# Optimization experiments

Measured on AMD Instinct MI355X. Metric: run time of the kernel, lower is better.

The kernel has to match this reference:

```python
import jax, jax.numpy as jnp
import numpy as np

B, S, D, H, FF = 4, 2048, 1024, 16, 4096
DT, TARGET, ITERS = 0.1, 0.0, 5


def _ln(x, w, b):
    mu = jnp.mean(x, axis=-1, keepdims=True)
    var = jnp.mean((x - mu) ** 2, axis=-1, keepdims=True)
    return (x - mu) * jax.lax.rsqrt(var + 1e-5) * w + b


def setup_inputs() -> dict:
    key = jax.random.key(0)
    ks = iter(jax.random.split(key, 16))
    w = lambda shape: jax.random.normal(next(ks), shape, dtype=jnp.float32) * 0.02
    return {
        "x": jax.random.normal(next(ks), (B, S, D), dtype=jnp.float32),
        "ln_attn_w": jnp.ones((D,), jnp.float32), "ln_attn_b": jnp.zeros((D,), jnp.float32),
        "attn_in_w": w((3 * D, D)), "attn_in_b": jnp.zeros((3 * D,), jnp.float32),
        "attn_out_w": w((D, D)), "attn_out_b": jnp.zeros((D,), jnp.float32),
        "ln1_w": jnp.ones((D,), jnp.float32), "ln1_b": jnp.zeros((D,), jnp.float32),
        "ln2_w": jnp.ones((D,), jnp.float32), "ln2_b": jnp.zeros((D,), jnp.float32),
        "inl_u_w": w((D, D)), "inl_u_b": jnp.zeros((D,), jnp.float32),
        "inl_a_w": w((D, D)), "inl_a_b": jnp.zeros((D,), jnp.float32),
        "inl_b_w": w((D, D)), "inl_b_b": jnp.zeros((D,), jnp.float32),
        "inl_g_w": w((D, D)), "inl_g_b": jnp.zeros((D,), jnp.float32),
        "ff1_w": w((FF, D)), "ff1_b": jnp.zeros((FF,), jnp.float32),
        "ff2_w": w((D, FF)), "ff2_b": jnp.zeros((D,), jnp.float32),
    }


def reference(x, ln_attn_w, ln_attn_b, attn_in_w, attn_in_b, attn_out_w, attn_out_b,
              ln1_w, ln1_b, ln2_w, ln2_b,
              inl_u_w, inl_u_b, inl_a_w, inl_a_b, inl_b_w, inl_b_b, inl_g_w, inl_g_b,
              ff1_w, ff1_b, ff2_w, ff2_b):
    dh = D // H
    scale = 1.0 / np.sqrt(dh).astype(np.float32)
    # --- causal multi-head attention (dropout = identity, eval mode) ---
    xn = _ln(x, ln_attn_w, ln_attn_b)
    qkv = xn @ attn_in_w.T + attn_in_b            # [B,S,3D]
    q, k, v = jnp.split(qkv, 3, axis=-1)
    hsplit = lambda t: t.reshape(B, S, H, dh).transpose(0, 2, 1, 3)  # [B,H,S,dh]
    q, k, v = hsplit(q), hsplit(k), hsplit(v)
    scores = jnp.einsum('bhqd,bhkd->bhqk', q, k) * scale
    causal = jnp.triu(jnp.ones((S, S), dtype=bool), 1)
    scores = jnp.where(causal, jnp.finfo(scores.dtype).min, scores)
    probs = jax.nn.softmax(scores, axis=-1)
    attn_out = jnp.einsum('bhqk,bhkd->bhqd', probs, v).transpose(0, 2, 1, 3).reshape(B, S, D)
    attn_out = attn_out @ attn_out_w.T + attn_out_b
    x = x + attn_out
    context = attn_out
    # --- INL integrator dynamics (controllers depend only on context) ---
    xs = _ln(x, ln1_w, ln1_b)
    vs = jnp.zeros_like(xs)
    u = context @ inl_u_w.T + inl_u_b
    alpha = jax.nn.sigmoid(context @ inl_a_w.T + inl_a_b)
    beta = jax.nn.softplus(context @ inl_b_w.T + inl_b_b)
    g = jax.nn.sigmoid(context @ inl_g_w.T + inl_g_b)
    for _ in range(ITERS):
        vs = vs + DT * (alpha * (TARGET - xs) - beta * vs + u)
        xs = xs + DT * g * vs
    x = x + xs
    # --- feed-forward (exact GELU as torch default) ---
    h = _ln(x, ln2_w, ln2_b)
    x = x + (jax.nn.gelu(h @ ff1_w.T + ff1_b, approximate=False) @ ff2_w.T + ff2_b)
    return x
```

## Files before the change

kernel.cpp:

```cpp
#include <hip/hip_runtime.h>
#include <cstdint>
#include <cmath>

typedef __attribute__((ext_vector_type(4))) float floatx4;
typedef __attribute__((ext_vector_type(8))) __bf16 bf16x8;
typedef __attribute__((ext_vector_type(4))) unsigned short ushort4v;

#define DEVI static __device__ __forceinline__

DEVI unsigned short f2b(float f) {
    unsigned x = __float_as_uint(f);
    return (unsigned short)((x + 0x7fffu + ((x >> 16) & 1u)) >> 16);
}
DEVI float b2f(unsigned short u) { return __uint_as_float(((unsigned)u) << 16); }

DEVI void load16(void* lds, const void* g) {
    __builtin_amdgcn_global_load_lds(
        (__attribute__((address_space(1))) void*)(const_cast<void*>(g)),
        (__attribute__((address_space(3))) void*)lds, 16, 0, 0);
}

DEVI floatx4 MFMA16(bf16x8 a, bf16x8 b, floatx4 c) {
    return __builtin_amdgcn_mfma_f32_16x16x32_bf16(a, b, c, 0, 0, 0);
}

__global__ __launch_bounds__(256) void cvt_all(const float* __restrict__ s0,
                                               const float* __restrict__ s1,
                                               const float* __restrict__ s2,
                                               const float* __restrict__ s3,
                                               const float* __restrict__ s4,
                                               const float* __restrict__ s5,
                                               const float* __restrict__ s6,
                                               const float* __restrict__ s7,
                                               unsigned short* d0, unsigned short* d1,
                                               unsigned short* d2, unsigned short* d3,
                                               unsigned short* d4, unsigned short* d5,
                                               unsigned short* d6, unsigned short* d7) {
    int i = blockIdx.x * 256 + threadIdx.x;
    int seg = i >> 18;
    int j = i & 262143;
    const float* src; unsigned short* dst;
    if (seg < 3)        { src = s0; dst = d0; j += seg * 262144; }
    else if (seg == 3)  { src = s1; dst = d1; }
    else if (seg == 4)  { src = s2; dst = d2; }
    else if (seg == 5)  { src = s3; dst = d3; }
    else if (seg == 6)  { src = s4; dst = d4; }
    else if (seg == 7)  { src = s5; dst = d5; }
    else if (seg < 12)  { src = s6; dst = d6; j += (seg - 8) * 262144; }
    else                { src = s7; dst = d7; j += (seg - 12) * 262144; }
    floatx4 v = ((const floatx4*)src)[j];
    ushort4v o;
    o[0] = f2b(v[0]); o[1] = f2b(v[1]); o[2] = f2b(v[2]); o[3] = f2b(v[3]);
    ((ushort4v*)dst)[j] = o;
}

__global__ __launch_bounds__(256) void catbias_kernel(const float* __restrict__ a,
                                                      const float* __restrict__ b,
                                                      const float* __restrict__ c,
                                                      const float* __restrict__ d,
                                                      float* __restrict__ o) {
    int i = blockIdx.x * 256 + threadIdx.x;
    int p = i >> 10, j = i & 1023;
    float v = (p == 0) ? a[j] : (p == 1) ? b[j] : (p == 2) ? c[j] : d[j];
    o[i] = v;
}

__global__ __launch_bounds__(256) void ln_kernel(const float* __restrict__ in,
                                                 const float* __restrict__ w,
                                                 const float* __restrict__ b,
                                                 unsigned short* __restrict__ obf) {
    const int row = blockIdx.x, tid = threadIdx.x;
    const floatx4* pr = (const floatx4*)(in + (size_t)row * 1024);
    floatx4 v = pr[tid];
    float s  = v[0] + v[1] + v[2] + v[3];
    float ss = v[0]*v[0] + v[1]*v[1] + v[2]*v[2] + v[3]*v[3];
    #pragma unroll
    for (int o = 32; o >= 1; o >>= 1) { s += __shfl_xor(s, o); ss += __shfl_xor(ss, o); }
    __shared__ float red[8];
    int wv = tid >> 6, lane = tid & 63;
    if (lane == 0) { red[wv] = s; red[4 + wv] = ss; }
    __syncthreads();
    s  = red[0] + red[1] + red[2] + red[3];
    ss = red[4] + red[5] + red[6] + red[7];
    float mu  = s * (1.0f / 1024.0f);
    float var = ss * (1.0f / 1024.0f) - mu * mu;
    float rstd = rsqrtf(var + 1e-5f);
    floatx4 wv4 = ((const floatx4*)w)[tid];
    floatx4 bv4 = ((const floatx4*)b)[tid];
    ushort4v t;
    #pragma unroll
    for (int c = 0; c < 4; c++) t[c] = f2b((v[c] - mu) * rstd * wv4[c] + bv4[c]);
    ((ushort4v*)(obf + (size_t)row * 1024))[tid] = t;
}

__global__ __launch_bounds__(256) void integrator_ln_kernel(const float* __restrict__ w1,
                                                            const float* __restrict__ b1,
                                                            const float* __restrict__ w2,
                                                            const float* __restrict__ b2,
                                                            const unsigned short* __restrict__ uabg,
                                                            float* __restrict__ xio,
                                                            unsigned short* __restrict__ hb) {
    const int row = blockIdx.x, tid = threadIdx.x;
    const int wv = tid >> 6, lane = tid & 63;
    __shared__ float red[8], red2[8];

    floatx4 v = ((const floatx4*)(xio + (size_t)row * 1024))[tid];
    float s  = v[0] + v[1] + v[2] + v[3];
    float ss = v[0]*v[0] + v[1]*v[1] + v[2]*v[2] + v[3]*v[3];
    #pragma unroll
    for (int o = 32; o >= 1; o >>= 1) { s += __shfl_xor(s, o); ss += __shfl_xor(ss, o); }
    if (lane == 0) { red[wv] = s; red[4 + wv] = ss; }
    __syncthreads();
    s  = red[0] + red[1] + red[2] + red[3];
    ss = red[4] + red[5] + red[6] + red[7];
    float mu  = s * (1.0f / 1024.0f);
    float rstd = rsqrtf(ss * (1.0f / 1024.0f) - mu * mu + 1e-5f);
    floatx4 w1v = ((const floatx4*)w1)[tid];
    floatx4 b1v = ((const floatx4*)b1)[tid];

    const unsigned short* ubase = uabg + (size_t)row * 4096 + tid * 4;
    ushort4v uu = *(const ushort4v*)(ubase);
    ushort4v aa = *(const ushort4v*)(ubase + 1024);
    ushort4v bb = *(const ushort4v*)(ubase + 2048);
    ushort4v gg = *(const ushort4v*)(ubase + 3072);
    floatx4 res;
    #pragma unroll
    for (int c = 0; c < 4; c++) {
        float xs = (v[c] - mu) * rstd * w1v[c] + b1v[c];
        float u = b2f(uu[c]), a = b2f(aa[c]), bt = b2f(bb[c]), g = b2f(gg[c]);
        float vs = 0.f;
        #pragma unroll
        for (int t = 0; t < 5; t++) {
            vs += 0.1f * (-a * xs - bt * vs + u);
            xs += 0.1f * g * vs;
        }
        res[c] = v[c] + xs;
    }
    ((floatx4*)(xio + (size_t)row * 1024))[tid] = res;

    float s2  = res[0] + res[1] + res[2] + res[3];
    float ss2 = res[0]*res[0] + res[1]*res[1] + res[2]*res[2] + res[3]*res[3];
    #pragma unroll
    for (int o = 32; o >= 1; o >>= 1) { s2 += __shfl_xor(s2, o); ss2 += __shfl_xor(ss2, o); }
    if (lane == 0) { red2[wv] = s2; red2[4 + wv] = ss2; }
    __syncthreads();
    s2  = red2[0] + red2[1] + red2[2] + red2[3];
    ss2 = red2[4] + red2[5] + red2[6] + red2[7];
    float mu2  = s2 * (1.0f / 1024.0f);
    float rstd2 = rsqrtf(ss2 * (1.0f / 1024.0f) - mu2 * mu2 + 1e-5f);
    floatx4 w2v = ((const floatx4*)w2)[tid];
    floatx4 b2v = ((const floatx4*)b2)[tid];
    ushort4v t;
    #pragma unroll
    for (int c = 0; c < 4; c++) t[c] = f2b((res[c] - mu2) * rstd2 * w2v[c] + b2v[c]);
    ((ushort4v*)(hb + (size_t)row * 1024))[tid] = t;
}

template <int EPI>
__global__ __launch_bounds__(256, 3) void gemm_bt(const unsigned short* __restrict__ A,
                                                  const unsigned short* __restrict__ W,
                                                  const float* __restrict__ bias, int K,
                                                  unsigned short* __restrict__ ob0,
                                                  unsigned short* __restrict__ ob1,
                                                  unsigned short* __restrict__ ob2,
                                                  float* __restrict__ of0,
                                                  const float* __restrict__ xres) {
    __shared__ unsigned short sA[3][128 * 32];
    __shared__ unsigned short sB[3][128 * 32];
    const int tid = threadIdx.x;
    const int wave = tid >> 6, lane = tid & 63;
    const int ln = lane & 15, quad = lane >> 4;
    const size_t m0 = (size_t)blockIdx.y * 128;
    const int n0 = blockIdx.x * 128;
    const int wm = (wave >> 1) * 64, wn = (wave & 1) * 64;

    const floatx4 z4 = {0.f, 0.f, 0.f, 0.f};
    floatx4 acc[4][4];
    #pragma unroll
    for (int mt = 0; mt < 4; mt++)
        #pragma unroll
        for (int nt = 0; nt < 4; nt++) acc[mt][nt] = z4;

    const int r16 = lane >> 2;
    const int gsw = (((lane & 3) ^ (r16 & 3) ^ ((r16 >> 2) & 3))) * 8;
    const int arow = wave * 16 + r16;
    const unsigned short* gA = A + (m0 + (size_t)arow) * K + gsw;
    const unsigned short* gB = W + ((size_t)(n0 + arow)) * K + gsw;
    const size_t rs64 = (size_t)64 * K;
    const int so = wave * 512;
    const int swr = ((quad ^ (ln & 3) ^ ((ln >> 2) & 3))) * 8;

    const int T = K >> 5;

    load16(&sA[0][so], gA);
    load16(&sA[0][so + 2048], gA + rs64);
    load16(&sB[0][so], gB);
    load16(&sB[0][so + 2048], gB + rs64);
    load16(&sA[1][so], gA + 32);
    load16(&sA[1][so + 2048], gA + rs64 + 32);
    load16(&sB[1][so], gB + 32);
    load16(&sB[1][so + 2048], gB + rs64 + 32);
    asm volatile("s_waitcnt vmcnt(4)" ::: "memory");
    asm volatile("s_barrier" ::: "memory");

    bf16x8 fa0[4], fb0[4], fa1[4], fb1[4];
    #pragma unroll
    for (int mt = 0; mt < 4; mt++)
        fa0[mt] = *(const bf16x8*)&sA[0][(wm + mt * 16 + ln) * 32 + swr];
    #pragma unroll
    for (int nt = 0; nt < 4; nt++)
        fb0[nt] = *(const bf16x8*)&sB[0][(wn + nt * 16 + ln) * 32 + swr];

    auto step = [&](int t, bf16x8* afc, bf16x8* bfc, bf16x8* afn, bf16x8* bfn) {
        if (t + 2 < T) {
            const int k = (t + 2) * 32;
            const int nb = (t + 2) % 3;
            load16(&sA[nb][so], gA + k);
            load16(&sA[nb][so + 2048], gA + rs64 + k);
            load16(&sB[nb][so], gB + k);
            load16(&sB[nb][so + 2048], gB + rs64 + k);
        }
        __builtin_amdgcn_sched_barrier(0);
        __builtin_amdgcn_s_setprio(1);
        #pragma unroll
        for (int mt = 0; mt < 4; mt++)
            #pragma unroll
            for (int nt = 0; nt < 4; nt++)
                acc[mt][nt] = MFMA16(afc[mt], bfc[nt], acc[mt][nt]);
        __builtin_amdgcn_s_setprio(0);
        __builtin_amdgcn_sched_barrier(0);
        if (t + 1 < T) {
            if (t + 2 < T) {
                asm volatile("s_waitcnt vmcnt(4) lgkmcnt(0)" ::: "memory");
            } else {
                asm volatile("s_waitcnt vmcnt(0) lgkmcnt(0)" ::: "memory");
            }
            asm volatile("s_barrier" ::: "memory");
            const int nb = (t + 1) % 3;
            afn[0] = *(const bf16x8*)&sA[nb][(wm + ln) * 32 + swr];
            #pragma unroll
            for (int nt = 0; nt < 4; nt++)
                bfn[nt] = *(const bf16x8*)&sB[nb][(wn + nt * 16 + ln) * 32 + swr];
            #pragma unroll
            for (int mt = 1; mt < 4; mt++)
                afn[mt] = *(const bf16x8*)&sA[nb][(wm + mt * 16 + ln) * 32 + swr];
        }
    };

    #pragma unroll 1
    for (int t = 0; t < T; t += 2) {
        step(t, fa0, fb0, fa1, fb1);
        step(t + 1, fa1, fb1, fa0, fb0);
    }

    const size_t rowb = m0 + wm + quad * 4;
    const int colb = n0 + wn + ln;
    #pragma unroll
    for (int mt = 0; mt < 4; mt++) {
        #pragma unroll
        for (int nt = 0; nt < 4; nt++) {
            const int n = colb + nt * 16;
            const float bs = bias[n];
            #pragma unroll
            for (int r = 0; r < 4; r++) {
                const size_t row = rowb + mt * 16 + r;
                float c = acc[mt][nt][r] + bs;
                if constexpr (EPI == 0) {
                    int sect = n >> 10, d1 = n & 1023, h = d1 >> 6, d = d1 & 63;
                    int bb = (int)(row >> 11), s = (int)(row & 2047);
                    size_t bh = (size_t)(bb * 16 + h);
                    if (sect == 0)      ob0[(bh * 2048 + s) * 64 + d] = f2b(c);
                    else if (sect == 1) ob1[(bh * 2048 + s) * 64 + d] = f2b(c);
                    else                ob2[(bh * 64 + d) * 2048 + s] = f2b(c);
                } else if constexpr (EPI == 1) {
                    size_t idx = row * 1024 + n;
                    ob0[idx] = f2b(c);
                    of0[idx] = xres[idx] + c;
                } else if constexpr (EPI == 2) {
                    int p = n >> 10;
                    float v;
                    if (p == 0)       v = c;
                    else if (p == 2)  v = fmaxf(c, 0.f) + log1pf(__expf(-fabsf(c)));
                    else              v = 1.f / (1.f + __expf(-c));
                    ob0[row * 4096 + n] = f2b(v);
                } else if constexpr (EPI == 3) {
                    float v = 0.5f * c * (1.f + erff(c * 0.70710678118654752f));
                    ob0[row * 4096 + n] = f2b(v);
                } else {
                    size_t idx = row * 1024 + n;
                    of0[idx] += c;
                }
            }
        }
    }
}

#define PSTR 72
__global__ __launch_bounds__(256, 3) void attn_kernel(const unsigned short* __restrict__ Qb,
                                                      const unsigned short* __restrict__ Kb,
                                                      const unsigned short* __restrict__ Vtb,
                                                      unsigned short* __restrict__ Ob) {
    __shared__ unsigned short sK[2][64 * 64];
    __shared__ unsigned short sVt[2][64 * 64];
    __shared__ unsigned short sQP[128 * PSTR];
    const int pr = blockIdx.x;
    const int bh = blockIdx.y;
    const int tid = threadIdx.x, wave = tid >> 6, lane = tid & 63;
    const int ln = lane & 15, quad = lane >> 4;
    const unsigned short* Q  = Qb  + (size_t)bh * 2048 * 64;
    const unsigned short* Kp = Kb  + (size_t)bh * 2048 * 64;
    const unsigned short* Vt = Vtb + (size_t)bh * 64 * 2048;

    const int rl  = lane >> 3;
    const int gsw = (((lane & 7) ^ rl)) * 8;
    const int sseg = wave * 2;
    const unsigned short* kbase = Kp + (size_t)(sseg * 8 + rl) * 64 + gsw;
    const unsigned short* vbase = Vt + (size_t)(sseg * 8 + rl) * 2048 + gsw;
    unsigned short* sP = &sQP[wave * 32 * PSTR];
    const int bb = bh >> 4, h = bh & 15;
    const floatx4 z4 = {0.f, 0.f, 0.f, 0.f};

    #pragma unroll 1
    for (int phase = 0; phase < 2; phase++) {
        const int qt = phase ? pr : (15 - pr);
        const int q0 = qt * 128;
        const int T = 2 * qt + 2;

        #pragma unroll
        for (int i = 0; i < 4; i++) {
            int s = wave * 4 + i;
            load16(&sQP[s * 512], Q + (size_t)(q0 + s * 8 + rl) * 64 + gsw);
        }
        load16(&sK[0][sseg * 512], kbase);
        load16(&sK[0][(sseg + 1) * 512], kbase + (size_t)8 * 64);
        load16(&sVt[0][sseg * 512], vbase);
        load16(&sVt[0][(sseg + 1) * 512], vbase + (size_t)8 * 2048);
        asm volatile("s_waitcnt vmcnt(0)" ::: "memory");
        asm volatile("s_barrier" ::: "memory");

        bf16x8 aq[2][2];
        #pragma unroll
        for (int mt = 0; mt < 2; mt++)
            #pragma unroll
            for (int ks = 0; ks < 2; ks++)
                aq[mt][ks] = *(const bf16x8*)&sQP[(wave * 32 + mt * 16 + ln) * 64 +
                                                  (((ks * 4 + quad) ^ (ln & 7)) * 8)];
        asm volatile("s_waitcnt lgkmcnt(0)" ::: "memory");
        asm volatile("s_barrier" ::: "memory");

        floatx4 Oacc[2][4];
        float m_run[2][4], l_run[2][4];
        #pragma unroll
        for (int mt = 0; mt < 2; mt++)
            #pragma unroll
            for (int j = 0; j < 4; j++) { Oacc[mt][j] = z4; m_run[mt][j] = -1e30f; l_run[mt][j] = 0.f; }

        const int wave_first = q0 + wave * 32;
        const int wave_last  = wave_first + 31;

        #pragma unroll 1
        for (int t = 0; t < T; t++) {
            const int kk0 = t * 64;
            const int cur = t & 1;
            if (t + 1 < T) {
                const unsigned short* kg = kbase + (size_t)(kk0 + 64) * 64;
                const unsigned short* vg = vbase + (size_t)(kk0 + 64);
                load16(&sK[cur ^ 1][sseg * 512], kg);
                load16(&sK[cur ^ 1][(sseg + 1) * 512], kg + (size_t)8 * 64);
                load16(&sVt[cur ^ 1][sseg * 512], vg);
                load16(&sVt[cur ^ 1][(sseg + 1) * 512], vg + (size_t)8 * 2048);
                asm volatile("s_waitcnt vmcnt(4)" ::: "memory");
            } else {
                asm volatile("s_waitcnt vmcnt(0)" ::: "memory");
            }
            asm volatile("s_barrier" ::: "memory");

            if (kk0 <= wave_last) {
                floatx4 Sc[2][4];
                #pragma unroll
                for (int mt = 0; mt < 2; mt++)
                    #pragma unroll
                    for (int nt = 0; nt < 4; nt++) Sc[mt][nt] = z4;
                __builtin_amdgcn_s_setprio(1);
                #pragma unroll
                for (int ks = 0; ks < 2; ks++) {
                    #pragma unroll
                    for (int nt = 0; nt < 4; nt++) {
                        bf16x8 bk = *(const bf16x8*)&sK[cur][(nt * 16 + ln) * 64 +
                                                             (((ks * 4 + quad) ^ (ln & 7)) * 8)];
                        #pragma unroll
                        for (int mt = 0; mt < 2; mt++)
                            Sc[mt][nt] = MFMA16(aq[mt][ks], bk, Sc[mt][nt]);
                    }
                }
                __builtin_amdgcn_s_setprio(0);
                const bool diag = (kk0 + 63 > wave_first);
                #pragma unroll
                for (int mt = 0; mt < 2; mt++)
                    #pragma unroll
                    for (int nt = 0; nt < 4; nt++)
                        #pragma unroll
                        for (int r = 0; r < 4; r++) {
                            float v = Sc[mt][nt][r] * 0.125f;
                            if (diag) {
                                int rowg = wave_first + mt * 16 + quad * 4 + r;
                                int colg = kk0 + nt * 16 + ln;
                                if (colg > rowg) v = -1e30f;
                            }
                            Sc[mt][nt][r] = v;
                        }
                float alpha[2][4];
                #pragma unroll
                for (int mt = 0; mt < 2; mt++)
                    #pragma unroll
                    for (int r = 0; r < 4; r++) {
                        float mx = fmaxf(fmaxf(Sc[mt][0][r], Sc[mt][1][r]), fmaxf(Sc[mt][2][r], Sc[mt][3][r]));
                        #pragma unroll
                        for (int off = 1; off < 16; off <<= 1) mx = fmaxf(mx, __shfl_xor(mx, off));
                        float mnew = fmaxf(m_run[mt][r], mx);
                        alpha[mt][r] = __expf(m_run[mt][r] - mnew);
                        m_run[mt][r] = mnew;
                    }
                #pragma unroll
                for (int mt = 0; mt < 2; mt++)
                    #pragma unroll
                    for (int r = 0; r < 4; r++) {
                        float rs = 0.f;
                        #pragma unroll
                        for (int nt = 0; nt < 4; nt++) {
                            float p = __expf(Sc[mt][nt][r] - m_run[mt][r]);
                            Sc[mt][nt][r] = p;
                            rs += p;
                        }
                        #pragma unroll
                        for (int off = 1; off < 16; off <<= 1) rs += __shfl_xor(rs, off);
                        l_run[mt][r] = l_run[mt][r] * alpha[mt][r] + rs;
                    }
                #pragma unroll
                for (int mt = 0; mt < 2; mt++)
                    #pragma unroll
                    for (int nt = 0; nt < 4; nt++)
                        #pragma unroll
                        for (int r = 0; r < 4; r++) Oacc[mt][nt][r] *= alpha[mt][r];
                #pragma unroll
                for (int mt = 0; mt < 2; mt++)
                    #pragma unroll
                    for (int nt = 0; nt < 4; nt++)
                        #pragma unroll
                        for (int r = 0; r < 4; r++)
                            sP[(mt * 16 + quad * 4 + r) * PSTR + nt * 16 + ln] = f2b(Sc[mt][nt][r]);
                __builtin_amdgcn_s_setprio(1);
                #pragma unroll
                for (int kp = 0; kp < 2; kp++) {
                    bf16x8 ap[2];
                    #pragma unroll
                    for (int mt = 0; mt < 2; mt++)
                        ap[mt] = *(const bf16x8*)&sP[(mt * 16 + ln) * PSTR + kp * 32 + quad * 8];
                    #pragma unroll
                    for (int nt = 0; nt < 4; nt++) {
                        bf16x8 bv = *(const bf16x8*)&sVt[cur][(nt * 16 + ln) * 64 +
                                                              (((kp * 4 + quad) ^ (ln & 7)) * 8)];
                        #pragma unroll
                        for (int mt = 0; mt < 2; mt++)
                            Oacc[mt][nt] = MFMA16(ap[mt], bv, Oacc[mt][nt]);
                    }
                }
                __builtin_amdgcn_s_setprio(0);
            }
            asm volatile("s_barrier" ::: "memory");
        }

        #pragma unroll
        for (int mt = 0; mt < 2; mt++)
            #pragma unroll
            for (int nt = 0; nt < 4; nt++)
                #pragma unroll
                for (int r = 0; r < 4; r++) {
                    float o = Oacc[mt][nt][r] / l_run[mt][r];
                    int srow = q0 + wave * 32 + mt * 16 + quad * 4 + r;
                    size_t tok = (size_t)bb * 2048 + srow;
                    Ob[tok * 1024 + h * 64 + nt * 16 + ln] = f2b(o);
                }
    }
}

extern "C" void kernel_launch(void* const* d_in, const int* in_sizes, int n_in,
                              void* d_out, int out_size, void* d_ws, size_t ws_size,
                              hipStream_t stream) {
    const float* x          = (const float*)d_in[0];
    const float* ln_attn_w  = (const float*)d_in[1];
    const float* ln_attn_b  = (const float*)d_in[2];
    const float* attn_in_w  = (const float*)d_in[3];
    const float* attn_in_b  = (const float*)d_in[4];
    const float* attn_out_w = (const float*)d_in[5];
    const float* attn_out_b = (const float*)d_in[6];
    const float* ln1_w      = (const float*)d_in[7];
    const float* ln1_b      = (const float*)d_in[8];
    const float* ln2_w      = (const float*)d_in[9];
    const float* ln2_b      = (const float*)d_in[10];
    const float* inl_u_w    = (const float*)d_in[11];
    const float* inl_u_b    = (const float*)d_in[12];
    const float* inl_a_w    = (const float*)d_in[13];
    const float* inl_a_b    = (const float*)d_in[14];
    const float* inl_b_w    = (const float*)d_in[15];
    const float* inl_b_b    = (const float*)d_in[16];
    const float* inl_g_w    = (const float*)d_in[17];
    const float* inl_g_b    = (const float*)d_in[18];
    const float* ff1_w      = (const float*)d_in[19];
    const float* ff1_b      = (const float*)d_in[20];
    const float* ff2_w      = (const float*)d_in[21];
    const float* ff2_b      = (const float*)d_in[22];
    float* out = (float*)d_out;

    char* ws = (char*)d_ws;
    unsigned short* Wqkv  = (unsigned short*)(ws);
    unsigned short* Wout  = (unsigned short*)(ws + 6291456);
    unsigned short* Winl  = (unsigned short*)(ws + 8388608);
    unsigned short* Wff1  = (unsigned short*)(ws + 16777216);
    unsigned short* Wff2  = (unsigned short*)(ws + 25165824);
    unsigned short* xnb   = (unsigned short*)(ws + 33554432);
    unsigned short* qb    = (unsigned short*)(ws + 50331648);
    unsigned short* kb    = (unsigned short*)(ws + 67108864);
    unsigned short* vtb   = (unsigned short*)(ws + 83886080);
    unsigned short* attnb = (unsigned short*)(ws + 100663296);
    unsigned short* ctxb  = (unsigned short*)(ws + 117440512);
    float*          bias4 = (float*)(ws + 167772160);
    unsigned short* uabg  = (unsigned short*)(ws + 50331648);
    unsigned short* ff1b  = (unsigned short*)(ws + 50331648);

    cvt_all<<<16384, 256, 0, stream>>>(attn_in_w, attn_out_w, inl_u_w, inl_a_w,
                                       inl_b_w, inl_g_w, ff1_w, ff2_w,
                                       Wqkv, Wout, Winl, Winl + 1048576,
                                       Winl + 2097152, Winl + 3145728, Wff1, Wff2);
    catbias_kernel<<<16, 256, 0, stream>>>(inl_u_b, inl_a_b, inl_b_b, inl_g_b, bias4);

    ln_kernel<<<8192, 256, 0, stream>>>(x, ln_attn_w, ln_attn_b, xnb);
    gemm_bt<0><<<dim3(24, 64), 256, 0, stream>>>(xnb, Wqkv, attn_in_b, 1024, qb, kb, vtb, nullptr, nullptr);
    attn_kernel<<<dim3(8, 64), 256, 0, stream>>>(qb, kb, vtb, attnb);
    gemm_bt<1><<<dim3(8, 64), 256, 0, stream>>>(attnb, Wout, attn_out_b, 1024, ctxb, nullptr, nullptr, out, x);
    gemm_bt<2><<<dim3(32, 64), 256, 0, stream>>>(ctxb, Winl, bias4, 1024, uabg, nullptr, nullptr, nullptr, nullptr);
    integrator_ln_kernel<<<8192, 256, 0, stream>>>(ln1_w, ln1_b, ln2_w, ln2_b, uabg, out, xnb);
    gemm_bt<3><<<dim3(32, 64), 256, 0, stream>>>(xnb, Wff1, ff1_b, 1024, ff1b, nullptr, nullptr, nullptr, nullptr);
    gemm_bt<4><<<dim3(8, 64), 256, 0, stream>>>(ff1b, Wff2, ff2_b, 4096, nullptr, nullptr, nullptr, out, nullptr);
}
```

Baseline: 860.2 us.

## Switch GEMM mainloop to BK=64 double-buffered LDS pipeline

The bf16 GEMM mainloop moves from a triple-buffered 32-wide K tile with register-fragment double buffering to a double-buffered 64-wide K tile. Each tile is consumed in two 32-wide halves, and the XOR swizzle is widened to 8 chunks. This halves the number of barriers per K and issues bigger global-to-LDS loads, with launch bounds lowered to 2 blocks per CU to fit the larger LDS. In exchange, fragment loads are no longer overlapped with MFMA, since each half waits on lgkmcnt(0) before computing, and occupancy drops.

```diff
diff --git a/kernel.cpp b/kernel.cpp
--- a/kernel.cpp
+++ b/kernel.cpp
@@ -157,7 +157,7 @@
 }
 
 template <int EPI>
-__global__ __launch_bounds__(256, 3) void gemm_bt(const unsigned short* __restrict__ A,
+__global__ __launch_bounds__(256, 2) void gemm_bt(const unsigned short* __restrict__ A,
                                                   const unsigned short* __restrict__ W,
                                                   const float* __restrict__ bias, int K,
                                                   unsigned short* __restrict__ ob0,
@@ -165,8 +165,8 @@
                                                   unsigned short* __restrict__ ob2,
                                                   float* __restrict__ of0,
                                                   const float* __restrict__ xres) {
-    __shared__ unsigned short sA[3][128 * 32];
-    __shared__ unsigned short sB[3][128 * 32];
+    __shared__ unsigned short sA[2][128 * 64];
+    __shared__ unsigned short sB[2][128 * 64];
     const int tid = threadIdx.x;
     const int wave = tid >> 6, lane = tid & 63;
     const int ln = lane & 15, quad = lane >> 4;
@@ -181,76 +181,69 @@
         #pragma unroll
         for (int nt = 0; nt < 4; nt++) acc[mt][nt] = z4;
 
-    const int r16 = lane >> 2;
-    const int gsw = (((lane & 3) ^ (r16 & 3) ^ ((r16 >> 2) & 3))) * 8;
-    const int arow = wave * 16 + r16;
-    const unsigned short* gA = A + (m0 + (size_t)arow) * K + gsw;
-    const unsigned short* gB = W + ((size_t)(n0 + arow)) * K + gsw;
-    const size_t rs64 = (size_t)64 * K;
-    const int so = wave * 512;
-    const int swr = ((quad ^ (ln & 3) ^ ((ln >> 2) & 3))) * 8;
-
-    const int T = K >> 5;
-
-    load16(&sA[0][so], gA);
-    load16(&sA[0][so + 2048], gA + rs64);
-    load16(&sB[0][so], gB);
-    load16(&sB[0][so + 2048], gB + rs64);
-    load16(&sA[1][so], gA + 32);
-    load16(&sA[1][so + 2048], gA + rs64 + 32);
-    load16(&sB[1][so], gB + 32);
-    load16(&sB[1][so + 2048], gB + rs64 + 32);
-    asm volatile("s_waitcnt vmcnt(4)" ::: "memory");
-    asm volatile("s_barrier" ::: "memory");
-
-    bf16x8 fa0[4], fb0[4], fa1[4], fb1[4];
-    #pragma unroll
-    for (int mt = 0; mt < 4; mt++)
-        fa0[mt] = *(const bf16x8*)&sA[0][(wm + mt * 16 + ln) * 32 + swr];
-    #pragma unroll
-    for (int nt = 0; nt < 4; nt++)
-        fb0[nt] = *(const bf16x8*)&sB[0][(wn + nt * 16 + ln) * 32 + swr];
-
-    auto step = [&](int t, bf16x8* afc, bf16x8* bfc, bf16x8* afn, bf16x8* bfn) {
-        if (t + 2 < T) {
-            const int k = (t + 2) * 32;
-            const int nb = (t + 2) % 3;
-            load16(&sA[nb][so], gA + k);
-            load16(&sA[nb][so + 2048], gA + rs64 + k);
-            load16(&sB[nb][so], gB + k);
-            load16(&sB[nb][so + 2048], gB + rs64 + k);
+    const int srow = tid >> 3;
+    const int ssw  = ((tid & 7) ^ (srow & 7)) * 8;
+    const unsigned short* gA = A + (m0 + srow) * K + ssw;
+    const unsigned short* gB = W + ((size_t)(n0 + srow)) * K + ssw;
+    const size_t rs32 = (size_t)32 * K;
+    const int lwb = wave * 512;
+
+    auto stage = [&](int buf, int t) {
+        const unsigned short* a = gA + (size_t)t * 64;
+        const unsigned short* b = gB + (size_t)t * 64;
+        #pragma unroll
+        for (int j = 0; j < 4; j++) {
+            load16(&sA[buf][j * 2048 + lwb], a + j * rs32);
+            load16(&sB[buf][j * 2048 + lwb], b + j * rs32);
         }
-        __builtin_amdgcn_sched_barrier(0);
+    };
+
+    const int lnx = ln & 7;
+    const int ga0 = (quad ^ lnx) * 8;
+    const int ga1 = ((quad + 4) ^ lnx) * 8;
+    bf16x8 fa[4], fb[4];
+    auto ldfrag = [&](int buf, int ga) {
+        #pragma unroll
+        for (int mt = 0; mt < 4; mt++)
+            fa[mt] = *(const bf16x8*)&sA[buf][(wm + mt * 16 + ln) * 64 + ga];
+        #pragma unroll
+        for (int nt = 0; nt < 4; nt++)
+            fb[nt] = *(const bf16x8*)&sB[buf][(wn + nt * 16 + ln) * 64 + ga];
+    };
+    auto mmah = [&]() {
         __builtin_amdgcn_s_setprio(1);
         #pragma unroll
         for (int mt = 0; mt < 4; mt++)
             #pragma unroll
             for (int nt = 0; nt < 4; nt++)
-                acc[mt][nt] = MFMA16(afc[mt], bfc[nt], acc[mt][nt]);
+                acc[mt][nt] = MFMA16(fa[mt], fb[nt], acc[mt][nt]);
         __builtin_amdgcn_s_setprio(0);
+    };
+
+    const int T = K >> 6;
+
+    stage(0, 0);
+    asm volatile("s_waitcnt vmcnt(0)" ::: "memory");
+    asm volatile("s_barrier" ::: "memory");
+
+    #pragma unroll 1
+    for (int t = 0; t < T; t++) {
+        const int c = t & 1;
+        if (t + 1 < T) stage(c ^ 1, t + 1);
+        __builtin_amdgcn_sched_barrier(0);
+        ldfrag(c, ga0);
+        asm volatile("s_waitcnt lgkmcnt(0)" ::: "memory");
+        __builtin_amdgcn_sched_barrier(0);
+        mmah();
+        ldfrag(c, ga1);
+        asm volatile("s_waitcnt lgkmcnt(0)" ::: "memory");
+        __builtin_amdgcn_sched_barrier(0);
+        mmah();
         __builtin_amdgcn_sched_barrier(0);
         if (t + 1 < T) {
-            if (t + 2 < T) {
-                asm volatile("s_waitcnt vmcnt(4) lgkmcnt(0)" ::: "memory");
-            } else {
-                asm volatile("s_waitcnt vmcnt(0) lgkmcnt(0)" ::: "memory");
-            }
+            asm volatile("s_waitcnt vmcnt(0)" ::: "memory");
             asm volatile("s_barrier" ::: "memory");
-            const int nb = (t + 1) % 3;
-            afn[0] = *(const bf16x8*)&sA[nb][(wm + ln) * 32 + swr];
-            #pragma unroll
-            for (int nt = 0; nt < 4; nt++)
-                bfn[nt] = *(const bf16x8*)&sB[nb][(wn + nt * 16 + ln) * 32 + swr];
-            #pragma unroll
-            for (int mt = 1; mt < 4; mt++)
-                afn[mt] = *(const bf16x8*)&sA[nb][(wm + mt * 16 + ln) * 32 + swr];
         }
-    };
-
-    #pragma unroll 1
-    for (int t = 0; t < T; t += 2) {
-        step(t, fa0, fb0, fa1, fb1);
-        step(t + 1, fa1, fb1, fa0, fb0);
     }
 
     const size_t rowb = m0 + wm + quad * 4;
```

Measured after the change: 825.9 us. 1.04x faster.

## Add dedicated K=64-tile double-buffered GEMM for the FF2 projection

Applied to the files above, without the earlier changes.

Replaces the generic 3-stage, K=32-tile GEMM used for the FF2 projection (K=4096) with a specialized kernel. The new kernel uses 64-wide K tiles, a double-buffered LDS pipeline with direct global-to-LDS loads, an XOR swizzle, and explicit waitcnt/barrier scheduling. It aims to halve the number of loop iterations and barriers across the long K dimension. In exchange it uses more LDS per block and lowers the occupancy hint from 3 to 2 blocks per CU.

```diff
diff --git a/kernel.cpp b/kernel.cpp
--- a/kernel.cpp
+++ b/kernel.cpp
@@ -157,14 +157,14 @@
 }
 
 template <int EPI>
-__global__ __launch_bounds__(256, 3) void gemm_bt(const unsigned short* __restrict__ A,
-                                                  const unsigned short* __restrict__ W,
-                                                  const float* __restrict__ bias, int K,
-                                                  unsigned short* __restrict__ ob0,
-                                                  unsigned short* __restrict__ ob1,
-                                                  unsigned short* __restrict__ ob2,
-                                                  float* __restrict__ of0,
-                                                  const float* __restrict__ xres) {
+__global__ __launch_bounds__(256, 3) void gemm32(const unsigned short* __restrict__ A,
+                                                 const unsigned short* __restrict__ W,
+                                                 const float* __restrict__ bias, int K,
+                                                 unsigned short* __restrict__ ob0,
+                                                 unsigned short* __restrict__ ob1,
+                                                 unsigned short* __restrict__ ob2,
+                                                 float* __restrict__ of0,
+                                                 const float* __restrict__ xres) {
     __shared__ unsigned short sA[3][128 * 32];
     __shared__ unsigned short sB[3][128 * 32];
     const int tid = threadIdx.x;
@@ -283,13 +283,112 @@
                     else if (p == 2)  v = fmaxf(c, 0.f) + log1pf(__expf(-fabsf(c)));
                     else              v = 1.f / (1.f + __expf(-c));
                     ob0[row * 4096 + n] = f2b(v);
-                } else if constexpr (EPI == 3) {
+                } else {
                     float v = 0.5f * c * (1.f + erff(c * 0.70710678118654752f));
                     ob0[row * 4096 + n] = f2b(v);
-                } else {
-                    size_t idx = row * 1024 + n;
-                    of0[idx] += c;
                 }
+            }
+        }
+    }
+}
+
+__global__ __launch_bounds__(256, 2) void gemm64_ff2(const unsigned short* __restrict__ A,
+                                                     const unsigned short* __restrict__ W,
+                                                     const float* __restrict__ bias, int K,
+                                                     float* __restrict__ of0) {
+    __shared__ unsigned short sA[2][128 * 64];
+    __shared__ unsigned short sB[2][128 * 64];
+    const int tid = threadIdx.x;
+    const int wave = tid >> 6, lane = tid & 63;
+    const int ln = lane & 15, quad = lane >> 4;
+    const size_t m0 = (size_t)blockIdx.y * 128;
+    const int n0 = blockIdx.x * 128;
+    const int wm = (wave >> 1) * 64, wn = (wave & 1) * 64;
+
+    const floatx4 z4 = {0.f, 0.f, 0.f, 0.f};
+    floatx4 acc[4][4];
+    #pragma unroll
+    for (int mt = 0; mt < 4; mt++)
+        #pragma unroll
+        for (int nt = 0; nt < 4; nt++) acc[mt][nt] = z4;
+
+    const int srow = tid >> 3;
+    const int ssw  = ((tid & 7) ^ (srow & 7)) * 8;
+    const unsigned short* gA = A + (m0 + srow) * K + ssw;
+    const unsigned short* gB = W + ((size_t)(n0 + srow)) * K + ssw;
+    const size_t rs32 = (size_t)32 * K;
+    const int lwb = wave * 512;
+
+    auto stage = [&](int buf, int t) {
+        const unsigned short* a = gA + (size_t)t * 64;
+        const unsigned short* b = gB + (size_t)t * 64;
+        #pragma unroll
+        for (int j = 0; j < 4; j++) {
+            load16(&sA[buf][j * 2048 + lwb], a + j * rs32);
+            load16(&sB[buf][j * 2048 + lwb], b + j * rs32);
+        }
+    };
+
+    const int lnx = ln & 7;
+    const int ga0 = (quad ^ lnx) * 8;
+    const int ga1 = ((quad + 4) ^ lnx) * 8;
+    bf16x8 fa[4], fb[4];
+    auto ldfrag = [&](int buf, int ga) {
+        #pragma unroll
+        for (int mt = 0; mt < 4; mt++)
+            fa[mt] = *(const bf16x8*)&sA[buf][(wm + mt * 16 + ln) * 64 + ga];
+        #pragma unroll
+        for (int nt = 0; nt < 4; nt++)
+            fb[nt] = *(const bf16x8*)&sB[buf][(wn + nt * 16 + ln) * 64 + ga];
+    };
+    auto mmah = [&]() {
+        __builtin_amdgcn_s_setprio(1);
+        #pragma unroll
+        for (int mt = 0; mt < 4; mt++)
+            #pragma unroll
+            for (int nt = 0; nt < 4; nt++)
+                acc[mt][nt] = MFMA16(fa[mt], fb[nt], acc[mt][nt]);
+        __builtin_amdgcn_s_setprio(0);
+    };
+
+    const int T = K >> 6;
+
+    stage(0, 0);
+    asm volatile("s_waitcnt vmcnt(0)" ::: "memory");
+    asm volatile("s_barrier" ::: "memory");
+
+    #pragma unroll 1
+    for (int t = 0; t < T; t++) {
+        const int c = t & 1;
+        if (t + 1 < T) stage(c ^ 1, t + 1);
+        __builtin_amdgcn_sched_barrier(0);
+        ldfrag(c, ga0);
+        asm volatile("s_waitcnt lgkmcnt(0)" ::: "memory");
+        __builtin_amdgcn_sched_barrier(0);
+        mmah();
+        ldfrag(c, ga1);
+        asm volatile("s_waitcnt lgkmcnt(0)" ::: "memory");
+        __builtin_amdgcn_sched_barrier(0);
+        mmah();
+        __builtin_amdgcn_sched_barrier(0);
+        if (t + 1 < T) {
+            asm volatile("s_waitcnt vmcnt(0)" ::: "memory");
+            asm volatile("s_barrier" ::: "memory");
+        }
+    }
+
+    const size_t rowb = m0 + wm + quad * 4;
+    const int colb = n0 + wn + ln;
+    #pragma unroll
+    for (int mt = 0; mt < 4; mt++) {
+        #pragma unroll
+        for (int nt = 0; nt < 4; nt++) {
+            const int n = colb + nt * 16;
+            const float bs = bias[n];
+            #pragma unroll
+            for (int r = 0; r < 4; r++) {
+                const size_t row = rowb + mt * 16 + r;
+                of0[row * 1024 + n] += acc[mt][nt][r] + bs;
             }
         }
     }
@@ -535,11 +634,11 @@
     catbias_kernel<<<16, 256, 0, stream>>>(inl_u_b, inl_a_b, inl_b_b, inl_g_b, bias4);
 
     ln_kernel<<<8192, 256, 0, stream>>>(x, ln_attn_w, ln_attn_b, xnb);
-    gemm_bt<0><<<dim3(24, 64), 256, 0, stream>>>(xnb, Wqkv, attn_in_b, 1024, qb, kb, vtb, nullptr, nullptr);
+    gemm32<0><<<dim3(24, 64), 256, 0, stream>>>(xnb, Wqkv, attn_in_b, 1024, qb, kb, vtb, nullptr, nullptr);
     attn_kernel<<<dim3(8, 64), 256, 0, stream>>>(qb, kb, vtb, attnb);
-    gemm_bt<1><<<dim3(8, 64), 256, 0, stream>>>(attnb, Wout, attn_out_b, 1024, ctxb, nullptr, nullptr, out, x);
-    gemm_bt<2><<<dim3(32, 64), 256, 0, stream>>>(ctxb, Winl, bias4, 1024, uabg, nullptr, nullptr, nullptr, nullptr);
+    gemm32<1><<<dim3(8, 64), 256, 0, stream>>>(attnb, Wout, attn_out_b, 1024, ctxb, nullptr, nullptr, out, x);
+    gemm32<2><<<dim3(32, 64), 256, 0, stream>>>(ctxb, Winl, bias4, 1024, uabg, nullptr, nullptr, nullptr, nullptr);
     integrator_ln_kernel<<<8192, 256, 0, stream>>>(ln1_w, ln1_b, ln2_w, ln2_b, uabg, out, xnb);
-    gemm_bt<3><<<dim3(32, 64), 256, 0, stream>>>(xnb, Wff1, ff1_b, 1024, ff1b, nullptr, nullptr, nullptr, nullptr);
-    gemm_bt<4><<<dim3(8, 64), 256, 0, stream>>>(ff1b, Wff2, ff2_b, 4096, nullptr, nullptr, nullptr, out, nullptr);
-}
+    gemm32<3><<<dim3(32, 64), 256, 0, stream>>>(xnb, Wff1, ff1_b, 1024, ff1b, nullptr, nullptr, nullptr, nullptr);
+    gemm64_ff2<<<dim3(8, 64), 256, 0, stream>>>(ff1b, Wff2, ff2_b, 4096, out);
+}
```

Result: faster. 794.0 us (-7.7%).
